# Performance work log

Hardware: AMD Instinct MI355X
Metric: run time of the kernel (lower is better)

## Reference

```python
import jax, jax.numpy as jnp
import numpy as np

DIM = 192; HEADS = 6; WS = 8; SHIFT = 4; HID = int(DIM * 4.0)
CAB_SCALE = 0.01; COMPRESS = 3; SQUEEZE = 30
B = 8; H0 = 128; W0 = 128


def window_partition(x, ws):
    Bn, H, W, C = x.shape
    x = x.reshape(Bn, H // ws, ws, W // ws, ws, C).transpose(0, 1, 3, 2, 4, 5)
    return x.reshape(-1, ws, ws, C)


def window_reverse(w, ws, H, W):
    Bn = w.shape[0] // ((H // ws) * (W // ws))
    x = w.reshape(Bn, H // ws, W // ws, ws, ws, -1).transpose(0, 1, 3, 2, 4, 5)
    return x.reshape(Bn, H, W, -1)


def layernorm(x, w, b):
    mu = jnp.mean(x, -1, keepdims=True)
    var = jnp.var(x, -1, keepdims=True)
    return (x - mu) * jax.lax.rsqrt(var + 1e-5) * w + b


def conv3x3(x, w, b):
    y = jax.lax.conv_general_dilated(x, w, (1, 1), [(1, 1), (1, 1)],
                                     dimension_numbers=('NCHW', 'OIHW', 'NCHW'))
    return y + b[None, :, None, None]


def _coords_table(ws):
    # continuous relative coords table, log-spaced as in SwinV2
    r = np.arange(-(ws - 1), ws, dtype=np.float32)
    t = np.stack(np.meshgrid(r, r, indexing='ij'), -1) / (ws - 1) * 8.0
    t = np.sign(t) * np.log2(np.abs(t) + 1.0) / np.log2(8.0)
    return jnp.asarray(t.reshape(-1, 2))  # ((2ws-1)^2, 2)


def _rel_index(ws):
    c = np.stack(np.meshgrid(np.arange(ws), np.arange(ws), indexing='ij')).reshape(2, -1)
    r = (c[:, :, None] - c[:, None, :]).transpose(1, 2, 0)
    r[..., 0] += ws - 1; r[..., 1] += ws - 1; r[..., 0] *= 2 * ws - 1
    return jnp.asarray(r.sum(-1))  # (N, N) int


def _attn_mask(H, W, ws, shift):
    img = np.zeros((1, H, W, 1), np.float32); cnt = 0
    for hs in (slice(0, -ws), slice(-ws, -shift), slice(-shift, None)):
        for wsl in (slice(0, -ws), slice(-ws, -shift), slice(-shift, None)):
            img[:, hs, wsl, :] = cnt; cnt += 1
    win = img.reshape(1, H // ws, ws, W // ws, ws, 1).transpose(0, 1, 3, 2, 4, 5).reshape(-1, ws * ws)
    m = win[:, None, :] - win[:, :, None]
    return jnp.asarray(np.where(m != 0, -100.0, 0.0).astype(np.float32))  # (nW, N, N)


def _forward(x, norm1_w, norm1_b, qkv_w, q_bias, v_bias, logit_scale,
             cpb_w1, cpb_b1, cpb_w2, proj_w, proj_b,
             cab1_w, cab1_b, cab2_w, cab2_b, ca1_w, ca1_b, ca2_w, ca2_b,
             norm2_w, norm2_b, fc1_w, fc1_b, fc2_w, fc2_b, H, W):
    Bn, L, C = x.shape
    nh = HEADS; hd = C // nh; N = WS * WS
    shortcut = x
    xn = layernorm(x, norm1_w, norm1_b)
    xi = xn.reshape(Bn, H, W, C)

    # ---- CAB branch (Conv-GELU-Conv + channel attention) ----
    xc = xi.transpose(0, 3, 1, 2)                      # NCHW
    c = conv3x3(xc, cab1_w, cab1_b)
    c = jax.nn.gelu(c, approximate=False)
    c = conv3x3(c, cab2_w, cab2_b)
    s = c.mean((2, 3))                                 # (B, C) squeeze
    s = jax.nn.relu(s @ ca1_w.T + ca1_b)
    s = jax.nn.sigmoid(s @ ca2_w.T + ca2_b)
    conv_x = (c * s[:, :, None, None]).transpose(0, 2, 3, 1).reshape(Bn, L, C)

    # ---- shifted-window cosine attention ----
    xs = jnp.roll(xi, (-SHIFT, -SHIFT), axis=(1, 2)) if SHIFT > 0 else xi
    xw = window_partition(xs, WS).reshape(-1, N, C)    # (B*nW, N, C)
    qkv_bias = jnp.concatenate([q_bias, jnp.zeros_like(v_bias), v_bias])
    qkv = (xw @ qkv_w.T + qkv_bias).reshape(-1, N, 3, nh, hd).transpose(2, 0, 3, 1, 4)
    q, k, v = qkv[0], qkv[1], qkv[2]                   # (B_, nh, N, hd)
    qn = q / jnp.maximum(jnp.linalg.norm(q, axis=-1, keepdims=True), 1e-12)
    kn = k / jnp.maximum(jnp.linalg.norm(k, axis=-1, keepdims=True), 1e-12)
    attn = jnp.einsum('bhnd,bhmd->bhnm', qn, kn)
    scale = jnp.exp(jnp.minimum(logit_scale, jnp.log(100.0)))  # (nh,1,1)
    attn = attn * scale
    # CPB MLP relative position bias
    hbias = jax.nn.relu(_coords_table(WS) @ cpb_w1.T + cpb_b1) @ cpb_w2.T  # (T, nh)
    rpb = hbias[_rel_index(WS).reshape(-1)].reshape(N, N, nh).transpose(2, 0, 1)
    attn = attn + 16.0 * jax.nn.sigmoid(rpb)[None]
    if SHIFT > 0:
        mask = _attn_mask(H, W, WS, SHIFT)             # (nW, N, N)
        nW = mask.shape[0]
        attn = (attn.reshape(-1, nW, nh, N, N) + mask[None, :, None]).reshape(-1, nh, N, N)
    attn = jax.nn.softmax(attn, axis=-1)
    out = jnp.einsum('bhnm,bhmd->bhnd', attn, v).transpose(0, 2, 1, 3).reshape(-1, N, C)
    out = out @ proj_w.T + proj_b
    out = window_reverse(out.reshape(-1, WS, WS, C), WS, H, W)
    if SHIFT > 0:
        out = jnp.roll(out, (SHIFT, SHIFT), axis=(1, 2))
    attn_x = out.reshape(Bn, L, C)

    x = shortcut + attn_x + CAB_SCALE * conv_x
    h = layernorm(x, norm2_w, norm2_b)
    h = jax.nn.gelu(h @ fc1_w.T + fc1_b, approximate=False) @ fc2_w.T + fc2_b
    return x + h


def setup_inputs() -> dict:
    key = jax.random.key(0)
    ks = jax.random.split(key, 24)
    r = lambda k, shp, s=0.02: (jax.random.normal(k, shp, jnp.float32) * s)
    C = DIM; Cc = DIM // COMPRESS; Cs = DIM // SQUEEZE
    return {
        'x': jax.random.normal(ks[0], (B, H0 * W0, C), jnp.float32),
        'H': H0, 'W': W0,
        'norm1_w': jnp.ones((C,), jnp.float32), 'norm1_b': jnp.zeros((C,), jnp.float32),
        'qkv_w': r(ks[1], (3 * C, C)),
        'q_bias': jnp.zeros((C,), jnp.float32), 'v_bias': jnp.zeros((C,), jnp.float32),
        'logit_scale': jnp.full((HEADS, 1, 1), np.log(10.0), jnp.float32),
        'cpb_w1': r(ks[2], (512, 2), 0.1), 'cpb_b1': jnp.zeros((512,), jnp.float32),
        'cpb_w2': r(ks[3], (HEADS, 512), 0.1),
        'proj_w': r(ks[4], (C, C)), 'proj_b': jnp.zeros((C,), jnp.float32),
        'cab1_w': r(ks[5], (Cc, C, 3, 3)), 'cab1_b': jnp.zeros((Cc,), jnp.float32),
        'cab2_w': r(ks[6], (C, Cc, 3, 3)), 'cab2_b': jnp.zeros((C,), jnp.float32),
        'ca1_w': r(ks[7], (Cs, C)), 'ca1_b': jnp.zeros((Cs,), jnp.float32),
        'ca2_w': r(ks[8], (C, Cs)), 'ca2_b': jnp.zeros((C,), jnp.float32),
        'norm2_w': jnp.ones((C,), jnp.float32), 'norm2_b': jnp.zeros((C,), jnp.float32),
        'fc1_w': r(ks[9], (HID, C)), 'fc1_b': jnp.zeros((HID,), jnp.float32),
        'fc2_w': r(ks[10], (C, HID)), 'fc2_b': jnp.zeros((C,), jnp.float32),
    }


def reference(x, H, W, norm1_w, norm1_b, qkv_w, q_bias, v_bias, logit_scale,
              cpb_w1, cpb_b1, cpb_w2, proj_w, proj_b,
              cab1_w, cab1_b, cab2_w, cab2_b, ca1_w, ca1_b, ca2_w, ca2_b,
              norm2_w, norm2_b, fc1_w, fc1_b, fc2_w, fc2_b):
    return _forward(x, norm1_w, norm1_b, qkv_w, q_bias, v_bias, logit_scale,
                    cpb_w1, cpb_b1, cpb_w2, proj_w, proj_b,
                    cab1_w, cab1_b, cab2_w, cab2_b, ca1_w, ca1_b, ca2_w, ca2_b,
                    norm2_w, norm2_b, fc1_w, fc1_b, fc2_w, fc2_b, int(H), int(W))
```

## Files before the change

kernel.cpp:

```cpp
#include <hip/hip_runtime.h>
#include <math.h>


typedef unsigned short u16;
typedef __attribute__((ext_vector_type(8))) short short8;
typedef __attribute__((ext_vector_type(4))) float f32x4;

#define DI static __device__ __forceinline__

DI float b2f(u16 u){ union{unsigned u; float f;} v; v.u = ((unsigned)u)<<16; return v.f; }
DI u16 f2b(float f){ union{float f; unsigned u;} v; v.f = f; unsigned r = v.u + 0x7fffu + ((v.u>>16)&1u); return (u16)(r>>16); }
DI float gelu_f(float x){
  const float u = x*(0.7978845608f + 0.0356774081f*x*x);
  const float r = __builtin_amdgcn_rcpf(1.0f + __expf(2.0f*u));
  return x - x*r;
}

#define C2PLANE (12582912L)

__global__ __launch_bounds__(256) void ln_k(const float* __restrict__ in,
    const float* __restrict__ w, const float* __restrict__ b, u16* __restrict__ out)
{
  const int row  = blockIdx.x*4 + (threadIdx.x>>6);
  const int lane = threadIdx.x & 63;
  const float* r = in + (long)row*192;
  float v0 = r[lane], v1 = r[lane+64], v2 = r[lane+128];
  float s = v0+v1+v2;
  #pragma unroll
  for (int m=1;m<64;m<<=1) s += __shfl_xor(s, m);
  float mu = s*(1.0f/192.0f);
  float d0=v0-mu, d1=v1-mu, d2=v2-mu;
  float q = d0*d0+d1*d1+d2*d2;
  #pragma unroll
  for (int m=1;m<64;m<<=1) q += __shfl_xor(q, m);
  float rstd = rsqrtf(q*(1.0f/192.0f)+1e-5f);
  u16* o = out + (long)row*192;
  o[lane]     = f2b(d0*rstd*w[lane]    +b[lane]);
  o[lane+64]  = f2b(d1*rstd*w[lane+64] +b[lane+64]);
  o[lane+128] = f2b(d2*rstd*w[lane+128]+b[lane+128]);
}

__global__ __launch_bounds__(256) void prep_k(
    const float* __restrict__ qkv_w, const float* __restrict__ q_bias,
    const float* __restrict__ v_bias, const float* __restrict__ proj_w,
    const float* __restrict__ fc1_w, const float* __restrict__ fc2_w,
    const float* __restrict__ cab1_w, const float* __restrict__ cab2_w,
    const float* __restrict__ lgs,
    float* __restrict__ qkvbias, u16* __restrict__ wqkv, u16* __restrict__ wproj,
    u16* __restrict__ wfc1, u16* __restrict__ wfc2, u16* __restrict__ wt1,
    u16* __restrict__ wt2, float* __restrict__ scale6)
{
  int o = blockIdx.x*256 + threadIdx.x;
  if (o < 576){ qkvbias[o] = (o<192)? q_bias[o] : ((o<384)? 0.f : v_bias[o-384]); return; }
  o -= 576;
  if (o < 110592){ wqkv[o] = f2b(qkv_w[o]); return; } o -= 110592;
  if (o < 36864){
    const int e = o&7, lane = (o>>3)&63, ks = (o>>9)%6, nr = o/3072;
    const int row = nr*16 + (lane&15), col = ks*32 + (lane>>4)*8 + e;
    wproj[o] = f2b(proj_w[row*192 + col]); return; } o -= 36864;
  if (o < 147456){
    const int e = o&7, lane = (o>>3)&63, ks = (o>>9)%6, rest = o/3072;
    const int nr = rest&3, p = rest>>2;
    const int row = p*64 + nr*16 + (lane&15), col = ks*32 + (lane>>4)*8 + e;
    wfc1[o] = f2b(fc1_w[row*192 + col]); return; } o -= 147456;
  if (o < 147456){
    const int e = o&7, lane = (o>>3)&63, ks2 = (o>>9)&1, rest = o>>10;
    const int nr2 = rest%12, p = rest/12;
    const int row = nr2*16 + (lane&15);
    const int col = p*64 + ks2*32 + (lane>>4)*8 + e;
    wfc2[o] = f2b(fc2_w[row*768 + col]); return; } o -= 147456;
  if (o < 110592){
    int s = o/12288, r = o%12288, oc = r/192, ic = r%192, kh = s/3, kw = s%3;
    wt1[o] = f2b(cab1_w[((oc*192+ic)*3+kh)*3+kw]); return; } o -= 110592;
  if (o < 110592){
    int s = o/12288, r = o%12288, oc = r/64, ic = r%64, kh = s/3, kw = s%3;
    wt2[o] = f2b(cab2_w[((oc*64+ic)*3+kh)*3+kw]); return; } o -= 110592;
  if (o < 6){ scale6[o] = expf(fminf(lgs[o], logf(100.f))); }
}

__global__ __launch_bounds__(256) void rpb_k(const float* __restrict__ w1,
    const float* __restrict__ b1, const float* __restrict__ w2, float* __restrict__ rpbL)
{
  __shared__ float hb[225*6];
  const int tid = threadIdx.x;
  if (tid < 225){
    int di = tid/15, dj = tid%15;
    float vi = (di-7)*(8.0f/7.0f), vj = (dj-7)*(8.0f/7.0f);
    float t0 = (vi==0.f)?0.f:copysignf(log2f(fabsf(vi)+1.f)*(1.f/3.f), vi);
    float t1 = (vj==0.f)?0.f:copysignf(log2f(fabsf(vj)+1.f)*(1.f/3.f), vj);
    float acc[6] = {0,0,0,0,0,0};
    for (int hd=0; hd<512; ++hd){
      float a = fmaxf(t0*w1[hd*2] + t1*w1[hd*2+1] + b1[hd], 0.f);
      #pragma unroll
      for (int h=0;h<6;++h) acc[h] += a*w2[h*512+hd];
    }
    #pragma unroll
    for (int h=0;h<6;++h) hb[tid*6+h] = acc[h];
  }
  __syncthreads();
  for (int o = tid; o < 24576; o += 256){
    int i = o&3, lane = (o>>2)&63, mK = (o>>8)&3, nQ = (o>>10)&3, h = o>>12;
    int q = nQ*16 + (lane&15), k = mK*16 + (lane>>4)*4 + i;
    int idx = ((q>>3)-(k>>3)+7)*15 + ((q&7)-(k&7)+7);
    rpbL[o] = 16.0f/(1.0f+expf(-hb[idx*6+h]));
  }
}

template<int EPI, int KK, int NN>
__global__ __launch_bounds__(256) void gemm4_k(
    const u16* __restrict__ A, const u16* __restrict__ W,
    const float* __restrict__ bias, u16* __restrict__ outb)
{
  constexpr int NP = NN/64;
  __shared__ __align__(16) u16 As[128*200];
  __shared__ __align__(16) u16 Bs[64*200];
  const int tid = threadIdx.x, w = tid>>6, lane = tid&63;
  const int fr = lane&15, g = lane>>4;
  const int m0 = blockIdx.x*128;
  u16* obuf = Bs;

  #pragma unroll
  for (int i=0;i<12;++i){ const int id=tid+i*256, row=id/24, cc=id%24;
    *(short8*)&As[row*200+cc*8] =
      *(const short8*)(A + (long)(m0+row)*KK + cc*8); }

  short8 breg[6];
  #define LOADB(p) { \
    _Pragma("unroll") \
    for (int i=0;i<6;++i){ const int id=tid+i*256, br=id/24, cc=id%24; \
      breg[i] = *(const short8*)(W + (long)((p)*64+br)*KK + cc*8); } }
  #define STOREB() { \
    _Pragma("unroll") \
    for (int i=0;i<6;++i){ const int id=tid+i*256, br=id/24, cc=id%24; \
      *(short8*)&Bs[br*200+cc*8] = breg[i]; } }

  LOADB(0);
  for (int p=0; p<NP; ++p){
    __syncthreads();
    STOREB();
    __syncthreads();
    if (p+1 < NP) LOADB(p+1);
    f32x4 acc[2][4];
    #pragma unroll
    for (int a=0;a<2;++a)
      #pragma unroll
      for (int b=0;b<4;++b) acc[a][b] = (f32x4){0.f,0.f,0.f,0.f};
    #pragma unroll
    for (int ks=0; ks<6; ++ks){
      short8 af0 = *(const short8*)&As[(w*32+   fr)*200 + ks*32 + g*8];
      short8 af1 = *(const short8*)&As[(w*32+16+fr)*200 + ks*32 + g*8];
      #pragma unroll
      for (int nr=0;nr<4;++nr){
        short8 bf = *(const short8*)&Bs[(nr*16+fr)*200 + ks*32 + g*8];
        acc[0][nr] = __builtin_amdgcn_mfma_f32_16x16x32_bf16(af0, bf, acc[0][nr], 0,0,0);
        acc[1][nr] = __builtin_amdgcn_mfma_f32_16x16x32_bf16(af1, bf, acc[1][nr], 0,0,0);
      } }
    __syncthreads();
    #pragma unroll
    for (int mr=0;mr<2;++mr)
      #pragma unroll
      for (int nr=0;nr<4;++nr){
        const float bc = bias[p*64+nr*16+fr];
        #pragma unroll
        for (int i=0;i<4;++i){
          const int tok = w*32+mr*16+g*4+i;
          obuf[tok*72 + nr*16+fr] = f2b(acc[mr][nr][i] + bc); } }
    __syncthreads();
    #pragma unroll
    for (int j=0;j<4;++j){
      const int idx = tid + j*256, tok = idx>>3, cc = idx&7;
      *(short8*)(outb + (long)(m0+tok)*NN + p*64 + cc*8) =
          *(const short8*)&obuf[tok*72 + cc*8]; }
  }
  #undef LOADB
  #undef STOREB
}

__global__ __launch_bounds__(256) void proj_k(
    const u16* __restrict__ A, const u16* __restrict__ W,
    const float* __restrict__ bias, const float* __restrict__ resx,
    const u16* __restrict__ c2in, const float* __restrict__ sgate,
    float* __restrict__ outf)
{
  __shared__ __align__(16) u16 As[64*200];
  const int tid = threadIdx.x, w = tid>>6, lane = tid&63;
  const int fr = lane&15, g = lane>>4;
  const int m0 = blockIdx.x*64;

  #pragma unroll
  for (int i=0;i<6;++i){ const int id=tid+i*256, r=id/24, cc=id%24;
    *(short8*)&As[r*200+cc*8] = *(const short8*)(A + (long)(m0+r)*192 + cc*8); }
  __syncthreads();

  f32x4 acc[12];
  #pragma unroll
  for (int n=0;n<12;++n) acc[n] = (f32x4){0.f,0.f,0.f,0.f};
  #pragma unroll
  for (int ks=0;ks<6;++ks){
    const short8 af = *(const short8*)&As[(w*16+fr)*200 + ks*32 + g*8];
    #pragma unroll
    for (int nr=0;nr<12;++nr){
      const short8 bf = *(const short8*)(W + ((nr*6+ks)*64 + lane)*8);
      acc[nr] = __builtin_amdgcn_mfma_f32_16x16x32_bf16(af, bf, acc[nr], 0,0,0);
    }
  }

  float* fbuf = (float*)As;
  #pragma unroll
  for (int ch=0;ch<2;++ch){
    __syncthreads();
    #pragma unroll
    for (int nr=0;nr<6;++nr){
      const float bc = bias[ch*96 + nr*16 + fr];
      #pragma unroll
      for (int i=0;i<4;++i)
        fbuf[(w*16+g*4+i)*100 + nr*16+fr] = acc[ch*6+nr][i] + bc;
    }
    __syncthreads();
    #pragma unroll
    for (int j=0;j<6;++j){
      const int idx = tid + j*256, t = idx/24, cc = idx%24;
      const int tokg = m0 + t, gc0 = ch*96 + cc*4;
      const long o = (long)tokg*192 + gc0;
      f32x4 v = *(const f32x4*)&fbuf[t*100 + cc*4];
      const f32x4 r = *(const f32x4*)(resx + o);
      const u16* cp = c2in + (long)ch*C2PLANE + (long)tokg*96 + cc*4;
      const float* sg = sgate + (tokg>>14)*192 + gc0;
      #pragma unroll
      for (int e=0;e<4;++e) v[e] += r[e] + 0.01f*b2f(cp[e])*sg[e];
      *(f32x4*)(outf + o) = v;
    }
  }
}

__global__ __launch_bounds__(256, 2) void mlp_k(
    const float* __restrict__ xio,
    const float* __restrict__ lw, const float* __restrict__ lb,
    const u16* __restrict__ w1, const float* __restrict__ b1,
    const u16* __restrict__ w2, const float* __restrict__ b2,
    float* __restrict__ out)
{
  __shared__ __align__(16) char SB[25600];
  const int tid = threadIdx.x, w = tid>>6, lane = tid&63;
  const int fr = lane&15, g = lane>>4;
  const int m0 = blockIdx.x*128;
  u16* hs = ((u16*)SB) + w*(32*72);

  short8 af[2][6];
  #pragma unroll
  for (int mr=0; mr<2; ++mr){
    const long r = (long)(m0 + w*32 + mr*16 + fr)*192;
    f32x4 v[6][2];
    float s = 0.f;
    #pragma unroll
    for (int ks=0; ks<6; ++ks){
      v[ks][0] = *(const f32x4*)(xio + r + ks*32 + g*8);
      v[ks][1] = *(const f32x4*)(xio + r + ks*32 + g*8 + 4);
      #pragma unroll
      for (int e=0;e<4;++e) s += v[ks][0][e] + v[ks][1][e];
    }
    s += __shfl_xor(s,16); s += __shfl_xor(s,32);
    const float mu = s*(1.0f/192.0f);
    float q = 0.f;
    #pragma unroll
    for (int ks=0; ks<6; ++ks)
      #pragma unroll
      for (int h=0;h<2;++h)
        #pragma unroll
        for (int e=0;e<4;++e){ const float d = v[ks][h][e]-mu; q += d*d; }
    q += __shfl_xor(q,16); q += __shfl_xor(q,32);
    const float rstd = rsqrtf(q*(1.0f/192.0f)+1e-5f);
    #pragma unroll
    for (int ks=0; ks<6; ++ks){
      const int c0 = ks*32 + g*8;
      #pragma unroll
      for (int h=0;h<2;++h)
        #pragma unroll
        for (int e=0;e<4;++e)
          af[mr][ks][h*4+e] =
            (short)f2b((v[ks][h][e]-mu)*rstd*lw[c0+h*4+e] + lb[c0+h*4+e]);
    }
  }

  f32x4 acc2[2][12];
  #pragma unroll
  for (int a=0;a<2;++a)
    #pragma unroll
    for (int n=0;n<12;++n) acc2[a][n] = (f32x4){0.f,0.f,0.f,0.f};

  for (int p=0; p<12; ++p){
    f32x4 a1[2][4];
    #pragma unroll
    for (int a=0;a<2;++a)
      #pragma unroll
      for (int n=0;n<4;++n) a1[a][n] = (f32x4){0.f,0.f,0.f,0.f};
    #pragma unroll
    for (int ks=0;ks<6;++ks){
      #pragma unroll
      for (int nr=0;nr<4;++nr){
        const short8 bf = *(const short8*)(w1 + ((((p*4+nr)*6+ks)<<6) + lane)*8);
        a1[0][nr] = __builtin_amdgcn_mfma_f32_16x16x32_bf16(af[0][ks], bf, a1[0][nr], 0,0,0);
        a1[1][nr] = __builtin_amdgcn_mfma_f32_16x16x32_bf16(af[1][ks], bf, a1[1][nr], 0,0,0);
      }
    }
    #pragma unroll
    for (int mr=0;mr<2;++mr)
      #pragma unroll
      for (int nr=0;nr<4;++nr){
        const float bc = b1[p*64 + nr*16 + fr];
        #pragma unroll
        for (int i=0;i<4;++i)
          hs[(mr*16+g*4+i)*72 + nr*16+fr] = f2b(gelu_f(a1[mr][nr][i] + bc));
      }
    #pragma unroll
    for (int ks2=0;ks2<2;++ks2){
      const short8 ah0 = *(const short8*)&hs[(fr   )*72 + ks2*32 + g*8];
      const short8 ah1 = *(const short8*)&hs[(16+fr)*72 + ks2*32 + g*8];
      #pragma unroll
      for (int nr2=0;nr2<12;++nr2){
        const short8 bf = *(const short8*)(w2 + ((((p*12+nr2)*2+ks2)<<6) + lane)*8);
        acc2[0][nr2] = __builtin_amdgcn_mfma_f32_16x16x32_bf16(ah0, bf, acc2[0][nr2], 0,0,0);
        acc2[1][nr2] = __builtin_amdgcn_mfma_f32_16x16x32_bf16(ah1, bf, acc2[1][nr2], 0,0,0);
      }
    }
  }

  float* fbuf = (float*)SB;
  #pragma unroll
  for (int hp=0; hp<2; ++hp){
    #pragma unroll
    for (int ch=0;ch<2;++ch){
      __syncthreads();
      if ((w>>1) == hp){
        #pragma unroll
        for (int mr=0;mr<2;++mr)
          #pragma unroll
          for (int nr=0;nr<6;++nr){
            const float bc = b2[ch*96 + nr*16 + fr];
            #pragma unroll
            for (int i=0;i<4;++i)
              fbuf[((w&1)*32+mr*16+g*4+i)*100 + nr*16+fr] = acc2[mr][ch*6+nr][i] + bc;
          }
      }
      __syncthreads();
      #pragma unroll
      for (int j=0;j<6;++j){
        const int idx = tid + j*256, t = idx/24, cc = idx%24;
        const long o = (long)(m0 + hp*64 + t)*192 + ch*96 + cc*4;
        f32x4 v = *(const f32x4*)&fbuf[t*100 + cc*4];
        const f32x4 r = *(const f32x4*)(xio + o);
        #pragma unroll
        for (int e=0;e<4;++e) v[e] += r[e];
        *(f32x4*)(out + o) = v;
      }
    }
  }
}

template<int EPI, int CG, int IC, int OCT, int OCP, int NR, int TG>
__global__ __launch_bounds__(256, 2) void conv4_k(
    const u16* __restrict__ A, const u16* __restrict__ Wt,
    const float* __restrict__ bias, u16* __restrict__ outb,
    float* __restrict__ ssum)
{
  constexpr int NTG = 9/TG, S = CG*NTG;
  constexpr int WN = (TG*OCP*4 + 255)/256;
  __shared__ __align__(16) u16 Ah[4*130*36];
  __shared__ __align__(16) u16 Wl[TG*OCP*36];
  const int tid = threadIdx.x, w = tid>>6, lane = tid&63;
  const int fr = lane&15, g = lane>>4;
  const int b = blockIdx.x>>6, y0 = (blockIdx.x&63)*2;
  const int oc0 = blockIdx.y*OCP;
  const int wrow = w>>1, wcol = (w&1)*64;

  f32x4 acc[4][NR];
  #pragma unroll
  for (int a=0;a<4;++a)
    #pragma unroll
    for (int n=0;n<NR;++n) acc[a][n] = (f32x4){0.f,0.f,0.f,0.f};

  short8 hreg[8], wreg[WN];

  #define PRELOAD(s) { \
    const int cg_=(s)/NTG, tg_=(s)%NTG; \
    if (tg_==0){ \
      _Pragma("unroll") \
      for (int i=0;i<8;++i){ \
        const int id=tid+i*256, p=id>>9, x=(id>>2)&127, cc=id&3, y=y0+p-1; \
        short8 v={0,0,0,0,0,0,0,0}; \
        if ((unsigned)y<128u) \
          v = *(const short8*)(A + (long)((((b<<7)|y)<<7)|x)*IC + cg_*32 + cc*8); \
        hreg[i]=v; } } \
    _Pragma("unroll") \
    for (int i=0;i<WN;++i){ \
      const int id=tid+i*256; \
      if (id < TG*OCP*4){ \
        const int t=id/(OCP*4), r=id%(OCP*4), oc=r>>2, cc=r&3; \
        wreg[i] = *(const short8*)(Wt + \
            (long)((tg_*TG+t)*OCT + oc0 + oc)*IC + cg_*32 + cc*8); } } }

  #define STORE_STAGED(s) { \
    const int tg_=(s)%NTG; \
    if (tg_==0){ \
      _Pragma("unroll") \
      for (int i=0;i<8;++i){ \
        const int id=tid+i*256, p=id>>9, x=(id>>2)&127, cc=id&3; \
        *(short8*)&Ah[(p*130 + x + 1)*36 + cc*8] = hreg[i]; } \
      if (tid < 32){ \
        const int p=tid>>3, r=tid&7, col=(r>>2)?129:0, cc=r&3; \
        *(short8*)&Ah[(p*130 + col)*36 + cc*8] = (short8){0,0,0,0,0,0,0,0}; } } \
    _Pragma("unroll") \
    for (int i=0;i<WN;++i){ \
      const int id=tid+i*256; \
      if (id < TG*OCP*4){ \
        const int t=id/(OCP*4), r=id%(OCP*4), oc=r>>2, cc=r&3; \
        *(short8*)&Wl[(t*OCP+oc)*36 + cc*8] = wreg[i]; } } }

  #define COMPUTE(s) { \
    const int tg_=(s)%NTG; \
    _Pragma("unroll") \
    for (int t=0;t<TG;++t){ \
      const int tap=tg_*TG+t, dy=tap/3, dx=tap%3; \
      short8 bf[NR]; \
      _Pragma("unroll") \
      for (int nr=0;nr<NR;++nr) \
        bf[nr] = *(const short8*)&Wl[(t*OCP + nr*16 + fr)*36 + g*8]; \
      short8 af2[4]; \
      _Pragma("unroll") \
      for (int mr=0;mr<4;++mr) \
        af2[mr] = *(const short8*)&Ah[((wrow+dy)*130 + wcol + mr*16 + fr + dx)*36 + g*8]; \
      _Pragma("unroll") \
      for (int mr=0;mr<4;++mr) \
        _Pragma("unroll") \
        for (int nr=0;nr<NR;++nr) \
          acc[mr][nr] = __builtin_amdgcn_mfma_f32_16x16x32_bf16(af2[mr], bf[nr], acc[mr][nr], 0,0,0); } }

  PRELOAD(0);
  for (int s=0; s<S; ++s){
    __syncthreads();
    STORE_STAGED(s);
    __syncthreads();
    if (s+1 < S) PRELOAD(s+1);
    COMPUTE(s);
  }
  #undef PRELOAD
  #undef STORE_STAGED
  #undef COMPUTE

  if constexpr (EPI==2){
    #pragma unroll
    for (int nr=0;nr<NR;++nr){
      const float bc = bias[oc0 + nr*16 + fr];
      float s = 0.f;
      #pragma unroll
      for (int mr=0;mr<4;++mr)
        #pragma unroll
        for (int i=0;i<4;++i) s += acc[mr][nr][i] + bc;
      s += __shfl_xor(s,16); s += __shfl_xor(s,32);
      if (lane < 16) atomicAdd(&ssum[b*192 + oc0 + nr*16 + lane], s);
    }
  }

  u16* ob = Ah;
  const long tb = (long)(((b<<7)|y0)<<7);
  __syncthreads();
  if constexpr (EPI==1){
    #pragma unroll
    for (int mr=0;mr<4;++mr)
      #pragma unroll
      for (int nr=0;nr<NR;++nr){
        const float bc = bias[nr*16 + fr];
        #pragma unroll
        for (int i=0;i<4;++i){
          const int tok = wrow*128 + wcol + mr*16 + g*4 + i;
          ob[tok*72 + nr*16+fr] = f2b(gelu_f(acc[mr][nr][i] + bc));
        }
      }
    __syncthreads();
    #pragma unroll
    for (int j=0;j<8;++j){
      const int idx = tid + j*256, tok = idx>>3, cc = idx&7;
      *(short8*)(outb + (tb+tok)*OCP + cc*8) = *(const short8*)&ob[tok*72 + cc*8];
    }
  } else {
    const long pbase = (long)blockIdx.y*C2PLANE;
    #pragma unroll
    for (int h=0;h<2;++h){
      if (h) __syncthreads();
      if (wrow == h){
        #pragma unroll
        for (int mr=0;mr<4;++mr)
          #pragma unroll
          for (int nr=0;nr<NR;++nr){
            const float bc = bias[oc0 + nr*16 + fr];
            #pragma unroll
            for (int i=0;i<4;++i){
              const int tok = wcol + mr*16 + g*4 + i;
              ob[tok*104 + nr*16+fr] = f2b(acc[mr][nr][i] + bc);
            }
          }
      }
      __syncthreads();
      #pragma unroll
      for (int j=0;j<6;++j){
        const int idx = tid + j*256, t = idx/12, cc = idx%12;
        *(short8*)(outb + pbase + (tb + h*128 + t)*96 + cc*8) =
            *(const short8*)&ob[t*104 + cc*8];
      }
    }
  }
}

__global__ __launch_bounds__(256) void se_k(const float* __restrict__ ssum,
    const float* __restrict__ ca1w, const float* __restrict__ ca1b,
    const float* __restrict__ ca2w, const float* __restrict__ ca2b,
    float* __restrict__ sgate)
{
  __shared__ float hid[48];
  const int tid = threadIdx.x;
  if (tid < 48){
    int b = tid/6, cs = tid%6;
    float a = ca1b[cs];
    for (int c=0;c<192;++c) a += ssum[b*192+c]*(1.f/16384.f)*ca1w[cs*192+c];
    hid[tid] = fmaxf(a, 0.f);
  }
  __syncthreads();
  for (int o = tid; o < 1536; o += 256){
    int b = o/192, c = o%192;
    float a = ca2b[c];
    #pragma unroll
    for (int cs=0;cs<6;++cs) a += hid[b*6+cs]*ca2w[c*6+cs];
    sgate[o] = 1.f/(1.f+expf(-a));
  }
}

__global__ __launch_bounds__(256) void attn_k(const u16* __restrict__ qkv,
    const float* __restrict__ rpbL, const float* __restrict__ scale6,
    u16* __restrict__ aout)
{
  __shared__ int  lidx_s[4][64];
  __shared__ char region_s[4][64];
  __shared__ __align__(16) u16 p_s[4][64*72];
  const int tid = threadIdx.x, w = tid>>6, lane = tid&63;
  const int task = blockIdx.x*4 + w;
  const int win = task/6, h = task - win*6;
  const int b = win>>8, wn = win&255, wy = wn>>4, wx = wn&15;
  {
    int i = lane>>3, j = lane&7;
    int hs = wy*8+i, ws = wx*8+j;
    lidx_s[w][lane] = (b<<14) | (((hs+4)&127)<<7) | ((ws+4)&127);
    int hb = hs<120?0:(hs<124?1:2), wb = ws<120?0:(ws<124?1:2);
    region_s[w][lane] = (char)(hb*3+wb);
  }
  __syncthreads();
  const int g = lane>>4, l15 = lane&15;
  const bool edge = (wy==15) || (wx==15);
  const float scl = scale6[h];
  const f32x4 zf = {0.f,0.f,0.f,0.f};

  short8 kf[4];
  #pragma unroll
  for (int mt=0; mt<4; ++mt){
    const long base = (long)lidx_s[w][mt*16+l15]*576 + 192 + h*32 + g*8;
    short8 r = *(const short8*)(qkv + base);
    float f[8]; float ss = 0.f;
    #pragma unroll
    for (int e=0;e<8;++e){ f[e] = b2f((u16)r[e]); ss += f[e]*f[e]; }
    ss += __shfl_xor(ss,16); ss += __shfl_xor(ss,32);
    const float inv = 1.0f/fmaxf(sqrtf(ss), 1e-12f);
    #pragma unroll
    for (int e=0;e<8;++e) kf[mt][e] = (short)f2b(f[e]*inv);
  }

  #pragma unroll
  for (int nt=0; nt<4; ++nt){
    short8 qf;
    {
      const long base = (long)lidx_s[w][nt*16+l15]*576 + h*32 + g*8;
      short8 r = *(const short8*)(qkv + base);
      float f[8]; float ss = 0.f;
      #pragma unroll
      for (int e=0;e<8;++e){ f[e] = b2f((u16)r[e]); ss += f[e]*f[e]; }
      ss += __shfl_xor(ss,16); ss += __shfl_xor(ss,32);
      const float inv = 1.0f/fmaxf(sqrtf(ss), 1e-12f);
      #pragma unroll
      for (int e=0;e<8;++e) qf[e] = (short)f2b(f[e]*inv);
    }
    f32x4 st[4];
    #pragma unroll
    for (int mt=0; mt<4; ++mt)
      st[mt] = __builtin_amdgcn_mfma_f32_16x16x32_bf16(kf[mt], qf, zf, 0, 0, 0);
    float lv[16];
    const float* rp = rpbL + ((h*4+nt)*4)*256 + lane*4;
    const int rq = edge ? region_s[w][nt*16+l15] : 0;
    #pragma unroll
    for (int mt=0; mt<4; ++mt){
      const f32x4 rb = *(const f32x4*)(rp + mt*256);
      #pragma unroll
      for (int i=0;i<4;++i){
        float v = st[mt][i]*scl + rb[i];
        if (edge && region_s[w][mt*16+g*4+i] != rq) v -= 100.0f;
        lv[mt*4+i] = v;
      }
    }
    float mx = lv[0];
    #pragma unroll
    for (int t=1;t<16;++t) mx = fmaxf(mx, lv[t]);
    mx = fmaxf(mx, __shfl_xor(mx,16)); mx = fmaxf(mx, __shfl_xor(mx,32));
    float sum = 0.f;
    #pragma unroll
    for (int t=0;t<16;++t){ lv[t] = __expf(lv[t]-mx); sum += lv[t]; }
    sum += __shfl_xor(sum,16); sum += __shfl_xor(sum,32);
    const float isum = 1.0f/sum;
    u16* pr = p_s[w] + (nt*16+l15)*72;
    #pragma unroll
    for (int mt=0; mt<4; ++mt){
      #pragma unroll
      for (int j=0;j<2;++j){
        unsigned lo = f2b(lv[mt*4+2*j]  *isum);
        unsigned hi = f2b(lv[mt*4+2*j+1]*isum);
        *(unsigned*)(pr + mt*16 + g*4 + 2*j) = lo | (hi<<16);
      }
    }
  }

  short8 vf[2][2];
  #pragma unroll
  for (int nd=0; nd<2; ++nd)
    #pragma unroll
    for (int kc=0; kc<2; ++kc)
      #pragma unroll
      for (int e=0;e<8;++e){
        const int tok = kc*32 + g*8 + e;
        vf[nd][kc][e] = (short)qkv[(long)lidx_s[w][tok]*576 + 384 + h*32 + nd*16 + l15];
      }

  __syncthreads();

  #pragma unroll
  for (int mt=0; mt<4; ++mt){
    const short8 a0 = *(const short8*)(p_s[w] + (mt*16+l15)*72 +      g*8);
    const short8 a1 = *(const short8*)(p_s[w] + (mt*16+l15)*72 + 32 + g*8);
    #pragma unroll
    for (int nd=0; nd<2; ++nd){
      f32x4 o = __builtin_amdgcn_mfma_f32_16x16x32_bf16(a0, vf[nd][0], zf, 0, 0, 0);
      o = __builtin_amdgcn_mfma_f32_16x16x32_bf16(a1, vf[nd][1], o, 0, 0, 0);
      #pragma unroll
      for (int i=0;i<4;++i){
        const int q = mt*16 + g*4 + i;
        aout[(long)lidx_s[w][q]*192 + h*32 + nd*16 + l15] = f2b(o[i]);
      }
    }
  }
}

extern "C" void kernel_launch(void* const* d_in, const int* in_sizes, int n_in,
                              void* d_out, int out_size, void* d_ws, size_t ws_size,
                              hipStream_t stream)
{
  const float* x     = (const float*)d_in[0];
  const float* n1w   = (const float*)d_in[3];
  const float* n1b   = (const float*)d_in[4];
  const float* qkvw  = (const float*)d_in[5];
  const float* qb    = (const float*)d_in[6];
  const float* vb    = (const float*)d_in[7];
  const float* lgs   = (const float*)d_in[8];
  const float* cpb1w = (const float*)d_in[9];
  const float* cpb1b = (const float*)d_in[10];
  const float* cpb2w = (const float*)d_in[11];
  const float* projw = (const float*)d_in[12];
  const float* projb = (const float*)d_in[13];
  const float* cab1w = (const float*)d_in[14];
  const float* cab1b = (const float*)d_in[15];
  const float* cab2w = (const float*)d_in[16];
  const float* cab2b = (const float*)d_in[17];
  const float* ca1w  = (const float*)d_in[18];
  const float* ca1b  = (const float*)d_in[19];
  const float* ca2w  = (const float*)d_in[20];
  const float* ca2b  = (const float*)d_in[21];
  const float* n2w   = (const float*)d_in[22];
  const float* n2b   = (const float*)d_in[23];
  const float* fc1w  = (const float*)d_in[24];
  const float* fc1b  = (const float*)d_in[25];
  const float* fc2w  = (const float*)d_in[26];
  const float* fc2b  = (const float*)d_in[27];
  float* dout = (float*)d_out;
  char* ws = (char*)d_ws;

  constexpr size_t OFF_XN  = 0;
  constexpr size_t OFF_G1  = 50331648;
  constexpr size_t OFF_C2  = 67108864;
  constexpr size_t OFF_AO  = 167772160;
  constexpr size_t OFF_QKV = 218103808;
  constexpr size_t OFF_SM  = 369098752;

  u16*   xn      = (u16*)(ws + OFF_XN);
  u16*   g1      = (u16*)(ws + OFF_G1);
  u16*   c2      = (u16*)(ws + OFF_C2);
  u16*   ao      = (u16*)(ws + OFF_AO);
  u16*   qkvb    = (u16*)(ws + OFF_QKV);
  float* qkvbias = (float*)(ws + OFF_SM);
  float* scale6  = (float*)(ws + OFF_SM + 4096);
  float* ssum    = (float*)(ws + OFF_SM + 8192);
  float* sgate   = (float*)(ws + OFF_SM + 16384);
  float* rpbL    = (float*)(ws + OFF_SM + 24576);
  u16*   wqkv    = (u16*)(ws + OFF_SM + 131072);
  u16*   wproj   = (u16*)(ws + OFF_SM + 360448);
  u16*   wfc1    = (u16*)(ws + OFF_SM + 434176);
  u16*   wfc2    = (u16*)(ws + OFF_SM + 729088);
  u16*   wt1     = (u16*)(ws + OFF_SM + 1024000);
  u16*   wt2     = (u16*)(ws + OFF_SM + 1245184);

  prep_k<<<2595, 256, 0, stream>>>(qkvw, qb, vb, projw, fc1w, fc2w, cab1w, cab2w,
                                   lgs, qkvbias, wqkv, wproj, wfc1, wfc2, wt1, wt2, scale6);
  rpb_k<<<1, 256, 0, stream>>>(cpb1w, cpb1b, cpb2w, rpbL);
  ln_k<<<32768, 256, 0, stream>>>(x, n1w, n1b, xn);
  hipMemsetAsync(ssum, 0, 1536*4, stream);
  conv4_k<1,6,192,64,64,4,9><<<dim3(512,1), 256, 0, stream>>>(xn, wt1, cab1b, g1, nullptr);
  conv4_k<2,2,64,192,96,6,3><<<dim3(512,2), 256, 0, stream>>>(g1, wt2, cab2b, c2, ssum);
  se_k<<<1, 256, 0, stream>>>(ssum, ca1w, ca1b, ca2w, ca2b, sgate);
  gemm4_k<0,192,576><<<1024, 256, 0, stream>>>(xn, wqkv, qkvbias, qkvb);
  attn_k<<<3072, 256, 0, stream>>>(qkvb, rpbL, scale6, ao);
  proj_k<<<2048, 256, 0, stream>>>(ao, wproj, projb, x, c2, sgate, dout);
  mlp_k<<<1024, 256, 0, stream>>>(dout, n2w, n2b, wfc1, fc1b, wfc2, fc2b, dout);
}
```

Baseline: 636.3 us.

## Merge first CAB conv and QKV GEMM into one heterogeneous launch

The first CAB 3x3 conv (512 blocks) and the QKV projection GEMM (1024 blocks) both read only the normalized input, so they are folded into a single kernel that dispatches on block index to either body, sharing one union LDS buffer. Running these independent stages together is meant to fill the GPU better than the small 512-block conv launch did alone, and to remove a launch boundary. In exchange the GEMM blocks now run under the conv's larger LDS footprint and the launch_bounds(256,2) register limit, which may lower their occupancy or cause register spills. proj_k and mlp_k are only moved in the file.

```diff
diff --git a/kernel.cpp b/kernel.cpp
--- a/kernel.cpp
+++ b/kernel.cpp
@@ -106,17 +106,17 @@
   }
 }
 
-template<int EPI, int KK, int NN>
-__global__ __launch_bounds__(256) void gemm4_k(
+template<int KK, int NN>
+DI void gemm4_body(char* LDSU, int bid, int tid,
     const u16* __restrict__ A, const u16* __restrict__ W,
     const float* __restrict__ bias, u16* __restrict__ outb)
 {
   constexpr int NP = NN/64;
-  __shared__ __align__(16) u16 As[128*200];
-  __shared__ __align__(16) u16 Bs[64*200];
-  const int tid = threadIdx.x, w = tid>>6, lane = tid&63;
+  u16* As = (u16*)LDSU;
+  u16* Bs = (u16*)(LDSU + 51200);
+  const int w = tid>>6, lane = tid&63;
   const int fr = lane&15, g = lane>>4;
-  const int m0 = blockIdx.x*128;
+  const int m0 = bid*128;
   u16* obuf = Bs;
 
   #pragma unroll
@@ -176,201 +176,20 @@
   #undef STOREB
 }
 
-__global__ __launch_bounds__(256) void proj_k(
-    const u16* __restrict__ A, const u16* __restrict__ W,
-    const float* __restrict__ bias, const float* __restrict__ resx,
-    const u16* __restrict__ c2in, const float* __restrict__ sgate,
-    float* __restrict__ outf)
-{
-  __shared__ __align__(16) u16 As[64*200];
-  const int tid = threadIdx.x, w = tid>>6, lane = tid&63;
-  const int fr = lane&15, g = lane>>4;
-  const int m0 = blockIdx.x*64;
-
-  #pragma unroll
-  for (int i=0;i<6;++i){ const int id=tid+i*256, r=id/24, cc=id%24;
-    *(short8*)&As[r*200+cc*8] = *(const short8*)(A + (long)(m0+r)*192 + cc*8); }
-  __syncthreads();
-
-  f32x4 acc[12];
-  #pragma unroll
-  for (int n=0;n<12;++n) acc[n] = (f32x4){0.f,0.f,0.f,0.f};
-  #pragma unroll
-  for (int ks=0;ks<6;++ks){
-    const short8 af = *(const short8*)&As[(w*16+fr)*200 + ks*32 + g*8];
-    #pragma unroll
-    for (int nr=0;nr<12;++nr){
-      const short8 bf = *(const short8*)(W + ((nr*6+ks)*64 + lane)*8);
-      acc[nr] = __builtin_amdgcn_mfma_f32_16x16x32_bf16(af, bf, acc[nr], 0,0,0);
-    }
-  }
-
-  float* fbuf = (float*)As;
-  #pragma unroll
-  for (int ch=0;ch<2;++ch){
-    __syncthreads();
-    #pragma unroll
-    for (int nr=0;nr<6;++nr){
-      const float bc = bias[ch*96 + nr*16 + fr];
-      #pragma unroll
-      for (int i=0;i<4;++i)
-        fbuf[(w*16+g*4+i)*100 + nr*16+fr] = acc[ch*6+nr][i] + bc;
-    }
-    __syncthreads();
-    #pragma unroll
-    for (int j=0;j<6;++j){
-      const int idx = tid + j*256, t = idx/24, cc = idx%24;
-      const int tokg = m0 + t, gc0 = ch*96 + cc*4;
-      const long o = (long)tokg*192 + gc0;
-      f32x4 v = *(const f32x4*)&fbuf[t*100 + cc*4];
-      const f32x4 r = *(const f32x4*)(resx + o);
-      const u16* cp = c2in + (long)ch*C2PLANE + (long)tokg*96 + cc*4;
-      const float* sg = sgate + (tokg>>14)*192 + gc0;
-      #pragma unroll
-      for (int e=0;e<4;++e) v[e] += r[e] + 0.01f*b2f(cp[e])*sg[e];
-      *(f32x4*)(outf + o) = v;
-    }
-  }
-}
-
-__global__ __launch_bounds__(256, 2) void mlp_k(
-    const float* __restrict__ xio,
-    const float* __restrict__ lw, const float* __restrict__ lb,
-    const u16* __restrict__ w1, const float* __restrict__ b1,
-    const u16* __restrict__ w2, const float* __restrict__ b2,
-    float* __restrict__ out)
-{
-  __shared__ __align__(16) char SB[25600];
-  const int tid = threadIdx.x, w = tid>>6, lane = tid&63;
-  const int fr = lane&15, g = lane>>4;
-  const int m0 = blockIdx.x*128;
-  u16* hs = ((u16*)SB) + w*(32*72);
-
-  short8 af[2][6];
-  #pragma unroll
-  for (int mr=0; mr<2; ++mr){
-    const long r = (long)(m0 + w*32 + mr*16 + fr)*192;
-    f32x4 v[6][2];
-    float s = 0.f;
-    #pragma unroll
-    for (int ks=0; ks<6; ++ks){
-      v[ks][0] = *(const f32x4*)(xio + r + ks*32 + g*8);
-      v[ks][1] = *(const f32x4*)(xio + r + ks*32 + g*8 + 4);
-      #pragma unroll
-      for (int e=0;e<4;++e) s += v[ks][0][e] + v[ks][1][e];
-    }
-    s += __shfl_xor(s,16); s += __shfl_xor(s,32);
-    const float mu = s*(1.0f/192.0f);
-    float q = 0.f;
-    #pragma unroll
-    for (int ks=0; ks<6; ++ks)
-      #pragma unroll
-      for (int h=0;h<2;++h)
-        #pragma unroll
-        for (int e=0;e<4;++e){ const float d = v[ks][h][e]-mu; q += d*d; }
-    q += __shfl_xor(q,16); q += __shfl_xor(q,32);
-    const float rstd = rsqrtf(q*(1.0f/192.0f)+1e-5f);
-    #pragma unroll
-    for (int ks=0; ks<6; ++ks){
-      const int c0 = ks*32 + g*8;
-      #pragma unroll
-      for (int h=0;h<2;++h)
-        #pragma unroll
-        for (int e=0;e<4;++e)
-          af[mr][ks][h*4+e] =
-            (short)f2b((v[ks][h][e]-mu)*rstd*lw[c0+h*4+e] + lb[c0+h*4+e]);
-    }
-  }
-
-  f32x4 acc2[2][12];
-  #pragma unroll
-  for (int a=0;a<2;++a)
-    #pragma unroll
-    for (int n=0;n<12;++n) acc2[a][n] = (f32x4){0.f,0.f,0.f,0.f};
-
-  for (int p=0; p<12; ++p){
-    f32x4 a1[2][4];
-    #pragma unroll
-    for (int a=0;a<2;++a)
-      #pragma unroll
-      for (int n=0;n<4;++n) a1[a][n] = (f32x4){0.f,0.f,0.f,0.f};
-    #pragma unroll
-    for (int ks=0;ks<6;++ks){
-      #pragma unroll
-      for (int nr=0;nr<4;++nr){
-        const short8 bf = *(const short8*)(w1 + ((((p*4+nr)*6+ks)<<6) + lane)*8);
-        a1[0][nr] = __builtin_amdgcn_mfma_f32_16x16x32_bf16(af[0][ks], bf, a1[0][nr], 0,0,0);
-        a1[1][nr] = __builtin_amdgcn_mfma_f32_16x16x32_bf16(af[1][ks], bf, a1[1][nr], 0,0,0);
-      }
-    }
-    #pragma unroll
-    for (int mr=0;mr<2;++mr)
-      #pragma unroll
-      for (int nr=0;nr<4;++nr){
-        const float bc = b1[p*64 + nr*16 + fr];
-        #pragma unroll
-        for (int i=0;i<4;++i)
-          hs[(mr*16+g*4+i)*72 + nr*16+fr] = f2b(gelu_f(a1[mr][nr][i] + bc));
-      }
-    #pragma unroll
-    for (int ks2=0;ks2<2;++ks2){
-      const short8 ah0 = *(const short8*)&hs[(fr   )*72 + ks2*32 + g*8];
-      const short8 ah1 = *(const short8*)&hs[(16+fr)*72 + ks2*32 + g*8];
-      #pragma unroll
-      for (int nr2=0;nr2<12;++nr2){
-        const short8 bf = *(const short8*)(w2 + ((((p*12+nr2)*2+ks2)<<6) + lane)*8);
-        acc2[0][nr2] = __builtin_amdgcn_mfma_f32_16x16x32_bf16(ah0, bf, acc2[0][nr2], 0,0,0);
-        acc2[1][nr2] = __builtin_amdgcn_mfma_f32_16x16x32_bf16(ah1, bf, acc2[1][nr2], 0,0,0);
-      }
-    }
-  }
-
-  float* fbuf = (float*)SB;
-  #pragma unroll
-  for (int hp=0; hp<2; ++hp){
-    #pragma unroll
-    for (int ch=0;ch<2;++ch){
-      __syncthreads();
-      if ((w>>1) == hp){
-        #pragma unroll
-        for (int mr=0;mr<2;++mr)
-          #pragma unroll
-          for (int nr=0;nr<6;++nr){
-            const float bc = b2[ch*96 + nr*16 + fr];
-            #pragma unroll
-            for (int i=0;i<4;++i)
-              fbuf[((w&1)*32+mr*16+g*4+i)*100 + nr*16+fr] = acc2[mr][ch*6+nr][i] + bc;
-          }
-      }
-      __syncthreads();
-      #pragma unroll
-      for (int j=0;j<6;++j){
-        const int idx = tid + j*256, t = idx/24, cc = idx%24;
-        const long o = (long)(m0 + hp*64 + t)*192 + ch*96 + cc*4;
-        f32x4 v = *(const f32x4*)&fbuf[t*100 + cc*4];
-        const f32x4 r = *(const f32x4*)(xio + o);
-        #pragma unroll
-        for (int e=0;e<4;++e) v[e] += r[e];
-        *(f32x4*)(out + o) = v;
-      }
-    }
-  }
-}
-
 template<int EPI, int CG, int IC, int OCT, int OCP, int NR, int TG>
-__global__ __launch_bounds__(256, 2) void conv4_k(
+DI void conv4_body(char* LDSU, int bx, int by, int tid,
     const u16* __restrict__ A, const u16* __restrict__ Wt,
     const float* __restrict__ bias, u16* __restrict__ outb,
     float* __restrict__ ssum)
 {
   constexpr int NTG = 9/TG, S = CG*NTG;
   constexpr int WN = (TG*OCP*4 + 255)/256;
-  __shared__ __align__(16) u16 Ah[4*130*36];
-  __shared__ __align__(16) u16 Wl[TG*OCP*36];
-  const int tid = threadIdx.x, w = tid>>6, lane = tid&63;
+  u16* Ah = (u16*)LDSU;
+  u16* Wl = (u16*)(LDSU + 37440);
+  const int w = tid>>6, lane = tid&63;
   const int fr = lane&15, g = lane>>4;
-  const int b = blockIdx.x>>6, y0 = (blockIdx.x&63)*2;
-  const int oc0 = blockIdx.y*OCP;
+  const int b = bx>>6, y0 = (bx&63)*2;
+  const int oc0 = by*OCP;
   const int wrow = w>>1, wcol = (w&1)*64;
 
   f32x4 acc[4][NR];
@@ -483,7 +302,7 @@
       *(short8*)(outb + (tb+tok)*OCP + cc*8) = *(const short8*)&ob[tok*72 + cc*8];
     }
   } else {
-    const long pbase = (long)blockIdx.y*C2PLANE;
+    const long pbase = (long)by*C2PLANE;
     #pragma unroll
     for (int h=0;h<2;++h){
       if (h) __syncthreads();
@@ -509,6 +328,30 @@
       }
     }
   }
+}
+
+__global__ __launch_bounds__(256, 2) void stage2_k(
+    const u16* __restrict__ xn, const u16* __restrict__ wt1,
+    const float* __restrict__ cab1b, u16* __restrict__ g1,
+    const u16* __restrict__ wqkv, const float* __restrict__ qkvbias,
+    u16* __restrict__ qkvb)
+{
+  __shared__ __align__(16) char LDSU[78912];
+  const int bid = blockIdx.x, tid = threadIdx.x;
+  if (bid < 512)
+    conv4_body<1,6,192,64,64,4,9>(LDSU, bid, 0, tid, xn, wt1, cab1b, g1, nullptr);
+  else
+    gemm4_body<192,576>(LDSU, bid-512, tid, xn, wqkv, qkvbias, qkvb);
+}
+
+__global__ __launch_bounds__(256, 2) void conv2_k(
+    const u16* __restrict__ g1, const u16* __restrict__ wt2,
+    const float* __restrict__ cab2b, u16* __restrict__ c2,
+    float* __restrict__ ssum)
+{
+  __shared__ __align__(16) char LDSU[58176];
+  conv4_body<2,2,64,192,96,6,3>(LDSU, blockIdx.x, blockIdx.y, threadIdx.x,
+                                g1, wt2, cab2b, c2, ssum);
 }
 
 __global__ __launch_bounds__(256) void se_k(const float* __restrict__ ssum,
@@ -649,6 +492,187 @@
       for (int i=0;i<4;++i){
         const int q = mt*16 + g*4 + i;
         aout[(long)lidx_s[w][q]*192 + h*32 + nd*16 + l15] = f2b(o[i]);
+      }
+    }
+  }
+}
+
+__global__ __launch_bounds__(256) void proj_k(
+    const u16* __restrict__ A, const u16* __restrict__ W,
+    const float* __restrict__ bias, const float* __restrict__ resx,
+    const u16* __restrict__ c2in, const float* __restrict__ sgate,
+    float* __restrict__ outf)
+{
+  __shared__ __align__(16) u16 As[64*200];
+  const int tid = threadIdx.x, w = tid>>6, lane = tid&63;
+  const int fr = lane&15, g = lane>>4;
+  const int m0 = blockIdx.x*64;
+
+  #pragma unroll
+  for (int i=0;i<6;++i){ const int id=tid+i*256, r=id/24, cc=id%24;
+    *(short8*)&As[r*200+cc*8] = *(const short8*)(A + (long)(m0+r)*192 + cc*8); }
+  __syncthreads();
+
+  f32x4 acc[12];
+  #pragma unroll
+  for (int n=0;n<12;++n) acc[n] = (f32x4){0.f,0.f,0.f,0.f};
+  #pragma unroll
+  for (int ks=0;ks<6;++ks){
+    const short8 af = *(const short8*)&As[(w*16+fr)*200 + ks*32 + g*8];
+    #pragma unroll
+    for (int nr=0;nr<12;++nr){
+      const short8 bf = *(const short8*)(W + ((nr*6+ks)*64 + lane)*8);
+      acc[nr] = __builtin_amdgcn_mfma_f32_16x16x32_bf16(af, bf, acc[nr], 0,0,0);
+    }
+  }
+
+  float* fbuf = (float*)As;
+  #pragma unroll
+  for (int ch=0;ch<2;++ch){
+    __syncthreads();
+    #pragma unroll
+    for (int nr=0;nr<6;++nr){
+      const float bc = bias[ch*96 + nr*16 + fr];
+      #pragma unroll
+      for (int i=0;i<4;++i)
+        fbuf[(w*16+g*4+i)*100 + nr*16+fr] = acc[ch*6+nr][i] + bc;
+    }
+    __syncthreads();
+    #pragma unroll
+    for (int j=0;j<6;++j){
+      const int idx = tid + j*256, t = idx/24, cc = idx%24;
+      const int tokg = m0 + t, gc0 = ch*96 + cc*4;
+      const long o = (long)tokg*192 + gc0;
+      f32x4 v = *(const f32x4*)&fbuf[t*100 + cc*4];
+      const f32x4 r = *(const f32x4*)(resx + o);
+      const u16* cp = c2in + (long)ch*C2PLANE + (long)tokg*96 + cc*4;
+      const float* sg = sgate + (tokg>>14)*192 + gc0;
+      #pragma unroll
+      for (int e=0;e<4;++e) v[e] += r[e] + 0.01f*b2f(cp[e])*sg[e];
+      *(f32x4*)(outf + o) = v;
+    }
+  }
+}
+
+__global__ __launch_bounds__(256, 2) void mlp_k(
+    const float* __restrict__ xio,
+    const float* __restrict__ lw, const float* __restrict__ lb,
+    const u16* __restrict__ w1, const float* __restrict__ b1,
+    const u16* __restrict__ w2, const float* __restrict__ b2,
+    float* __restrict__ out)
+{
+  __shared__ __align__(16) char SB[25600];
+  const int tid = threadIdx.x, w = tid>>6, lane = tid&63;
+  const int fr = lane&15, g = lane>>4;
+  const int m0 = blockIdx.x*128;
+  u16* hs = ((u16*)SB) + w*(32*72);
+
+  short8 af[2][6];
+  #pragma unroll
+  for (int mr=0; mr<2; ++mr){
+    const long r = (long)(m0 + w*32 + mr*16 + fr)*192;
+    f32x4 v[6][2];
+    float s = 0.f;
+    #pragma unroll
+    for (int ks=0; ks<6; ++ks){
+      v[ks][0] = *(const f32x4*)(xio + r + ks*32 + g*8);
+      v[ks][1] = *(const f32x4*)(xio + r + ks*32 + g*8 + 4);
+      #pragma unroll
+      for (int e=0;e<4;++e) s += v[ks][0][e] + v[ks][1][e];
+    }
+    s += __shfl_xor(s,16); s += __shfl_xor(s,32);
+    const float mu = s*(1.0f/192.0f);
+    float q = 0.f;
+    #pragma unroll
+    for (int ks=0; ks<6; ++ks)
+      #pragma unroll
+      for (int h=0;h<2;++h)
+        #pragma unroll
+        for (int e=0;e<4;++e){ const float d = v[ks][h][e]-mu; q += d*d; }
+    q += __shfl_xor(q,16); q += __shfl_xor(q,32);
+    const float rstd = rsqrtf(q*(1.0f/192.0f)+1e-5f);
+    #pragma unroll
+    for (int ks=0; ks<6; ++ks){
+      const int c0 = ks*32 + g*8;
+      #pragma unroll
+      for (int h=0;h<2;++h)
+        #pragma unroll
+        for (int e=0;e<4;++e)
+          af[mr][ks][h*4+e] =
+            (short)f2b((v[ks][h][e]-mu)*rstd*lw[c0+h*4+e] + lb[c0+h*4+e]);
+    }
+  }
+
+  f32x4 acc2[2][12];
+  #pragma unroll
+  for (int a=0;a<2;++a)
+    #pragma unroll
+    for (int n=0;n<12;++n) acc2[a][n] = (f32x4){0.f,0.f,0.f,0.f};
+
+  for (int p=0; p<12; ++p){
+    f32x4 a1[2][4];
+    #pragma unroll
+    for (int a=0;a<2;++a)
+      #pragma unroll
+      for (int n=0;n<4;++n) a1[a][n] = (f32x4){0.f,0.f,0.f,0.f};
+    #pragma unroll
+    for (int ks=0;ks<6;++ks){
+      #pragma unroll
+      for (int nr=0;nr<4;++nr){
+        const short8 bf = *(const short8*)(w1 + ((((p*4+nr)*6+ks)<<6) + lane)*8);
+        a1[0][nr] = __builtin_amdgcn_mfma_f32_16x16x32_bf16(af[0][ks], bf, a1[0][nr], 0,0,0);
+        a1[1][nr] = __builtin_amdgcn_mfma_f32_16x16x32_bf16(af[1][ks], bf, a1[1][nr], 0,0,0);
+      }
+    }
+    #pragma unroll
+    for (int mr=0;mr<2;++mr)
+      #pragma unroll
+      for (int nr=0;nr<4;++nr){
+        const float bc = b1[p*64 + nr*16 + fr];
+        #pragma unroll
+        for (int i=0;i<4;++i)
+          hs[(mr*16+g*4+i)*72 + nr*16+fr] = f2b(gelu_f(a1[mr][nr][i] + bc));
+      }
+    #pragma unroll
+    for (int ks2=0;ks2<2;++ks2){
+      const short8 ah0 = *(const short8*)&hs[(fr   )*72 + ks2*32 + g*8];
+      const short8 ah1 = *(const short8*)&hs[(16+fr)*72 + ks2*32 + g*8];
+      #pragma unroll
+      for (int nr2=0;nr2<12;++nr2){
+        const short8 bf = *(const short8*)(w2 + ((((p*12+nr2)*2+ks2)<<6) + lane)*8);
+        acc2[0][nr2] = __builtin_amdgcn_mfma_f32_16x16x32_bf16(ah0, bf, acc2[0][nr2], 0,0,0);
+        acc2[1][nr2] = __builtin_amdgcn_mfma_f32_16x16x32_bf16(ah1, bf, acc2[1][nr2], 0,0,0);
+      }
+    }
+  }
+
+  float* fbuf = (float*)SB;
+  #pragma unroll
+  for (int hp=0; hp<2; ++hp){
+    #pragma unroll
+    for (int ch=0;ch<2;++ch){
+      __syncthreads();
+      if ((w>>1) == hp){
+        #pragma unroll
+        for (int mr=0;mr<2;++mr)
+          #pragma unroll
+          for (int nr=0;nr<6;++nr){
+            const float bc = b2[ch*96 + nr*16 + fr];
+            #pragma unroll
+            for (int i=0;i<4;++i)
+              fbuf[((w&1)*32+mr*16+g*4+i)*100 + nr*16+fr] = acc2[mr][ch*6+nr][i] + bc;
+          }
+      }
+      __syncthreads();
+      #pragma unroll
+      for (int j=0;j<6;++j){
+        const int idx = tid + j*256, t = idx/24, cc = idx%24;
+        const long o = (long)(m0 + hp*64 + t)*192 + ch*96 + cc*4;
+        f32x4 v = *(const f32x4*)&fbuf[t*100 + cc*4];
+        const f32x4 r = *(const f32x4*)(xio + o);
+        #pragma unroll
+        for (int e=0;e<4;++e) v[e] += r[e];
+        *(f32x4*)(out + o) = v;
       }
     }
   }
@@ -716,10 +740,9 @@
   rpb_k<<<1, 256, 0, stream>>>(cpb1w, cpb1b, cpb2w, rpbL);
   ln_k<<<32768, 256, 0, stream>>>(x, n1w, n1b, xn);
   hipMemsetAsync(ssum, 0, 1536*4, stream);
-  conv4_k<1,6,192,64,64,4,9><<<dim3(512,1), 256, 0, stream>>>(xn, wt1, cab1b, g1, nullptr);
-  conv4_k<2,2,64,192,96,6,3><<<dim3(512,2), 256, 0, stream>>>(g1, wt2, cab2b, c2, ssum);
+  stage2_k<<<1536, 256, 0, stream>>>(xn, wt1, cab1b, g1, wqkv, qkvbias, qkvb);
+  conv2_k<<<dim3(512,2), 256, 0, stream>>>(g1, wt2, cab2b, c2, ssum);
   se_k<<<1, 256, 0, stream>>>(ssum, ca1w, ca1b, ca2w, ca2b, sgate);
-  gemm4_k<0,192,576><<<1024, 256, 0, stream>>>(xn, wqkv, qkvbias, qkvb);
   attn_k<<<3072, 256, 0, stream>>>(qkvb, rpbL, scale6, ao);
   proj_k<<<2048, 256, 0, stream>>>(ao, wproj, projb, x, c2, sgate, dout);
   mlp_k<<<1024, 256, 0, stream>>>(dout, n2w, n2b, wfc1, fc1b, wfc2, fc2b, dout);
```

After: 801.6 us. 1.26x slower.
